# Performance work log

Hardware: AMD Instinct MI355X
Metric: run time of the kernel (lower is better)

## Reference

```python
import jax, jax.numpy as jnp
import numpy as np

B, H, S, W, F = 16, 4, 8, 256, 16


def setup_inputs() -> dict:
    key = jax.random.key(0)
    kx, kk = jax.random.split(key)
    x = jax.random.normal(kx, (B, S, W, F), dtype=jnp.float32)
    kernel = jax.random.normal(kk, (H, S, S, W), dtype=jnp.float32)
    return {"x": x, "kernel": kernel}


def reference(x, kernel):
    # kernel: [H, S, S, W]; x: [B, S, W, F]
    Hh, Ss, _, Ww = kernel.shape
    r = jnp.arange(Ww)
    # stacked[h,x,y,j,i] = roll(kernel, shifts=j+1)[i] = kernel[(i-(j+1)) % W]
    idx = (r[None, :] - (r[:, None] + 1)) % Ww          # [W(row=j), W(col=i)]
    stacked = kernel[..., idx]                            # [H,S,S,W,W]
    # torch.tril over last two dims: keep col i <= row j
    tri = (r[None, :] <= r[:, None])                      # [W,W]
    stacked = jnp.where(tri, stacked, jnp.zeros((), dtype=stacked.dtype))
    # masked triangular time-mix contraction
    out = jnp.einsum('hxyji,bxif->bhxyjf', stacked, x)    # [B,H,S,S,W,F]
    base = jnp.arange(1, Ww + 1, dtype=out.dtype).reshape(1, 1, 1, 1, Ww, 1)
    out = out / base
    # transform_x: on diagonal series (x==y) roll time dim by 1, zero first step
    diag_mod = jnp.roll(out, 1, axis=4)
    not_first = (r != 0).reshape(1, 1, 1, 1, Ww, 1)
    diag_mod = diag_mod * not_first.astype(out.dtype)
    eye = jnp.eye(Ss, dtype=bool).reshape(1, 1, Ss, Ss, 1, 1)
    return jnp.where(eye, diag_mod, out)
```

## Files before the change

kernel.cpp:

```cpp
#include <hip/hip_runtime.h>
#include <hip/hip_bf16.h>

typedef short short8 __attribute__((ext_vector_type(8)));
typedef float f32x4 __attribute__((ext_vector_type(4)));

union FragAB { unsigned long long l[2]; int i[4]; short8 v; };

__global__ __launch_bounds__(256, 3)
void k_fused(const float* __restrict__ x,
             const float* __restrict__ kern,
             float* __restrict__ out)
{
    __shared__ __align__(16) ushort Xts[64 * 264];
    __shared__ __align__(8)  ushort wforL[4][336];
    __shared__ float rtab[256];

    const int blk = blockIdx.x;
    const int hy = blk & 31;
    const int sx = (blk >> 5) & 7;
    const int nt = blk >> 8;
    const int h = hy >> 3, sy = hy & 7;
    const int diag = (sx == sy) ? 1 : 0;
    const int t = threadIdx.x;

    {
        const float* krow = kern + ((h * 8 + sx) * 8 + sy) * 256;
        float v = krow[t];
        __hip_bfloat16 hv = __float2bfloat16(v);
        ushort u = reinterpret_cast<ushort&>(hv);
        #pragma unroll
        for (int s = 0; s < 4; ++s)
            wforL[s][t + s] = u;
        if (t < 88) {
            #pragma unroll
            for (int s = 0; s < 4; ++s) {
                int q = 256 + s + t;
                if (q < 336) wforL[s][q] = 0;
            }
        }
        if (t < 4) {
            #pragma unroll
            for (int s = 1; s < 4; ++s)
                if (t < s) wforL[s][t] = 0;
        }
    }
    {
        int denom = t + 1 - diag;
        rtab[t] = (denom > 0) ? (1.0f / (float)denom) : 0.0f;
    }
    {
        const float4* xbase = reinterpret_cast<const float4*>(x);
        #pragma unroll
        for (int it = 0; it < 8; ++it) {
            int id = it * 256 + t;
            int fq = id & 3;
            int k2 = (id >> 2) & 127;
            int bl = id >> 9;
            const float4* rowp = xbase + ((size_t)((nt * 4 + bl) * 8 + sx)) * 1024;
            float4 a = rowp[(2 * k2) * 4 + fq];
            float4 cq = rowp[(2 * k2 + 1) * 4 + fq];
            #pragma unroll
            for (int e = 0; e < 4; ++e) {
                float va = (&a.x)[e], vb = (&cq.x)[e];
                __hip_bfloat16 ha = __float2bfloat16(va);
                __hip_bfloat16 hb = __float2bfloat16(vb);
                uint u = (uint)reinterpret_cast<ushort&>(ha) |
                         ((uint)reinterpret_cast<ushort&>(hb) << 16);
                int row = bl * 16 + fq * 4 + e;
                *reinterpret_cast<uint*>(reinterpret_cast<char*>(Xts) + row * 528 + k2 * 4) = u;
            }
        }
    }
    __syncthreads();

    const int lane = t & 63, wid = t >> 6;
    const int laneM = lane & 15, laneG = lane >> 4;
    const int wj0 = wid * 64;
    const int kmax = wj0 + 64;

    const char* XtsB = reinterpret_cast<const char*>(Xts);
    const char* WB = reinterpret_cast<const char*>(wforL);
    const int abyte = laneM * 528 + laneG * 16;

    const int w00 = 255 + diag - wj0 - laneM + 8 * laneG;
    const int s = (laneM - diag + 1) & 3;
    const int bB = s * 674 + 2 * w00;

    f32x4 acc[4][4];
    #pragma unroll
    for (int m = 0; m < 4; ++m)
        #pragma unroll
        for (int n = 0; n < 4; ++n)
            acc[m][n] = (f32x4){0.0f, 0.0f, 0.0f, 0.0f};

    for (int kc = 0; kc < kmax; kc += 32) {
        FragAB af[4];
        #pragma unroll
        for (int m = 0; m < 4; ++m) {
            const int4 raw = *reinterpret_cast<const int4*>(XtsB + abyte + m * 8448 + kc * 2);
            af[m].i[0] = raw.x; af[m].i[1] = raw.y;
            af[m].i[2] = raw.z; af[m].i[3] = raw.w;
        }
        FragAB bf[4];
        #pragma unroll
        for (int n = 0; n < 4; ++n) {
            const char* p = WB + bB + kc * 2 - 32 * n;
            bf[n].l[0] = *reinterpret_cast<const unsigned long long*>(p);
            bf[n].l[1] = *reinterpret_cast<const unsigned long long*>(p + 8);
        }
        #pragma unroll
        for (int m = 0; m < 4; ++m)
            #pragma unroll
            for (int n = 0; n < 4; ++n)
                acc[m][n] = __builtin_amdgcn_mfma_f32_16x16x32_bf16(
                    af[m].v, bf[n].v, acc[m][n], 0, 0, 0);
    }

    #pragma unroll
    for (int m = 0; m < 4; ++m) {
        const int b_ = nt * 4 + m;
        float* obase = out + (((size_t)(b_ * 4 + h) * 8 + sx) * 8 + sy) * 4096
                       + laneG * 4;
        #pragma unroll
        for (int n = 0; n < 4; ++n) {
            const int j = wj0 + 16 * n + laneM;
            const float rt = rtab[j];
            f32x4 v = acc[m][n] * rt;
            __builtin_nontemporal_store(
                v, reinterpret_cast<f32x4*>(obase + (size_t)j * 16));
        }
    }
}

extern "C" void kernel_launch(void* const* d_in, const int* in_sizes, int n_in,
                              void* d_out, int out_size, void* d_ws, size_t ws_size,
                              hipStream_t stream) {
    const float* x    = (const float*)d_in[0];
    const float* kern = (const float*)d_in[1];
    float* out = (float*)d_out;

    k_fused<<<1024, 256, 0, stream>>>(x, kern, out);
}
```

Baseline: 19.75 us.

## Split x bf16 conversion into prep kernel, read MFMA A fragments from global

Adds a prep kernel that converts x to bf16 once and writes it to workspace in a layout matching the MFMA A-fragment order. The main kernel no longer stages x into shared memory and loads A fragments directly from global memory, which removes the redundant per-block conversion (x was reconverted by 32 blocks each) and the large shared allocation. The cost is an extra kernel launch plus uncached-ish global loads inside the MFMA loop instead of LDS reads. The occupancy hint is also dropped.

```diff
diff --git a/kernel.cpp b/kernel.cpp
--- a/kernel.cpp
+++ b/kernel.cpp
@@ -6,13 +6,54 @@
 
 union FragAB { unsigned long long l[2]; int i[4]; short8 v; };
 
-__global__ __launch_bounds__(256, 3)
-void k_fused(const float* __restrict__ x,
-             const float* __restrict__ kern,
-             float* __restrict__ out)
+
+__global__ __launch_bounds__(256)
+void k_prep(const float* __restrict__ x, ushort* __restrict__ xTf)
 {
-    __shared__ __align__(16) ushort Xts[64 * 264];
-    __shared__ __align__(8)  ushort wforL[4][336];
+    __shared__ float xs[256 * 17];
+    const int blk = blockIdx.x;
+    const int b = blk >> 3, sx = blk & 7;
+    const int t = threadIdx.x;
+
+    const float4* src = reinterpret_cast<const float4*>(x + (b * 8 + sx) * 4096);
+    #pragma unroll
+    for (int it = 0; it < 4; ++it) {
+        int id = it * 256 + t;
+        float4 v = src[id];
+        int k = id >> 2, fq = (id & 3) * 4;
+        xs[k * 17 + fq + 0] = v.x;
+        xs[k * 17 + fq + 1] = v.y;
+        xs[k * 17 + fq + 2] = v.z;
+        xs[k * 17 + fq + 3] = v.w;
+    }
+    __syncthreads();
+
+    const int f = t >> 4, kh = t & 15;
+    #pragma unroll
+    for (int d = 0; d < 2; ++d) {
+        const int kb = 2 * kh + d;
+        uint u[4];
+        #pragma unroll
+        for (int i = 0; i < 4; ++i) {
+            float v0 = xs[(kb * 8 + 2 * i) * 17 + f];
+            float v1 = xs[(kb * 8 + 2 * i + 1) * 17 + f];
+            __hip_bfloat16 h0 = __float2bfloat16(v0);
+            __hip_bfloat16 h1 = __float2bfloat16(v1);
+            u[i] = (uint)reinterpret_cast<ushort&>(h0) |
+                   ((uint)reinterpret_cast<ushort&>(h1) << 16);
+        }
+        int4* dst = reinterpret_cast<int4*>(
+            xTf + ((size_t)(sx * 32 + kb) * 256 + b * 16 + f) * 8);
+        *dst = make_int4((int)u[0], (int)u[1], (int)u[2], (int)u[3]);
+    }
+}
+
+__global__ __launch_bounds__(256)
+void k_main(const ushort* __restrict__ xTf,
+            const float* __restrict__ kern,
+            float* __restrict__ out)
+{
+    __shared__ __align__(8) ushort wforL[4][336];
     __shared__ float rtab[256];
 
     const int blk = blockIdx.x;
@@ -43,33 +84,8 @@
             for (int s = 1; s < 4; ++s)
                 if (t < s) wforL[s][t] = 0;
         }
-    }
-    {
         int denom = t + 1 - diag;
         rtab[t] = (denom > 0) ? (1.0f / (float)denom) : 0.0f;
-    }
-    {
-        const float4* xbase = reinterpret_cast<const float4*>(x);
-        #pragma unroll
-        for (int it = 0; it < 8; ++it) {
-            int id = it * 256 + t;
-            int fq = id & 3;
-            int k2 = (id >> 2) & 127;
-            int bl = id >> 9;
-            const float4* rowp = xbase + ((size_t)((nt * 4 + bl) * 8 + sx)) * 1024;
-            float4 a = rowp[(2 * k2) * 4 + fq];
-            float4 cq = rowp[(2 * k2 + 1) * 4 + fq];
-            #pragma unroll
-            for (int e = 0; e < 4; ++e) {
-                float va = (&a.x)[e], vb = (&cq.x)[e];
-                __hip_bfloat16 ha = __float2bfloat16(va);
-                __hip_bfloat16 hb = __float2bfloat16(vb);
-                uint u = (uint)reinterpret_cast<ushort&>(ha) |
-                         ((uint)reinterpret_cast<ushort&>(hb) << 16);
-                int row = bl * 16 + fq * 4 + e;
-                *reinterpret_cast<uint*>(reinterpret_cast<char*>(Xts) + row * 528 + k2 * 4) = u;
-            }
-        }
     }
     __syncthreads();
 
@@ -78,9 +94,9 @@
     const int wj0 = wid * 64;
     const int kmax = wj0 + 64;
 
-    const char* XtsB = reinterpret_cast<const char*>(Xts);
     const char* WB = reinterpret_cast<const char*>(wforL);
-    const int abyte = laneM * 528 + laneG * 16;
+    const ushort* agbase = xTf + ((size_t)(sx * 32 + laneG) * 256
+                                  + nt * 64 + laneM) * 8;
 
     const int w00 = 255 + diag - wj0 - laneM + 8 * laneG;
     const int s = (laneM - diag + 1) & 3;
@@ -97,7 +113,8 @@
         FragAB af[4];
         #pragma unroll
         for (int m = 0; m < 4; ++m) {
-            const int4 raw = *reinterpret_cast<const int4*>(XtsB + abyte + m * 8448 + kc * 2);
+            const int4 raw = *reinterpret_cast<const int4*>(
+                agbase + ((size_t)(kc >> 3) * 256 + 16 * m) * 8);
             af[m].i[0] = raw.x; af[m].i[1] = raw.y;
             af[m].i[2] = raw.z; af[m].i[3] = raw.w;
         }
@@ -138,6 +155,8 @@
     const float* x    = (const float*)d_in[0];
     const float* kern = (const float*)d_in[1];
     float* out = (float*)d_out;
+    ushort* xTf = (ushort*)d_ws;
 
-    k_fused<<<1024, 256, 0, stream>>>(x, kern, out);
+    k_prep<<<128, 256, 0, stream>>>(x, xTf);
+    k_main<<<1024, 256, 0, stream>>>(xTf, kern, out);
 }
```

After: 24.75 us. 1.25x slower.
